# Kernel optimization log

Hardware: AMD Instinct MI355X
Metric: run time of the kernel (lower is better)

## Reference

```python
import math
import jax, jax.numpy as jnp
import numpy as np

D_MODEL = 512
NHEAD = 8
D_HEAD = D_MODEL // NHEAD
ATTN_TEMP = 1.0
B, LQ, LK = 2, 2048, 4096


def _linear_params(key, d_in, d_out):
    kw, kb = jax.random.split(key)
    bound = 1.0 / math.sqrt(d_in)
    W = jax.random.uniform(kw, (d_out, d_in), jnp.float32, -bound, bound)
    b = jax.random.uniform(kb, (d_out,), jnp.float32, -bound, bound)
    return W, b


def setup_inputs() -> dict:
    key = jax.random.key(0)
    ks = jax.random.split(key, 8)
    q = jax.random.normal(ks[0], (B, LQ, D_MODEL), jnp.float32)
    kv = jax.random.normal(ks[1], (B, LK, D_MODEL), jnp.float32)
    key_gate = jax.random.uniform(ks[2], (B, LK), jnp.float32)
    key_mask = jax.random.randint(ks[3], (B, LK), 0, 2, jnp.int32)
    Wq, bq = _linear_params(ks[4], D_MODEL, D_MODEL)
    Wk, bk = _linear_params(ks[5], D_MODEL, D_MODEL)
    Wv, bv = _linear_params(ks[6], D_MODEL, D_MODEL)
    Wo, bo = _linear_params(ks[7], D_MODEL, D_MODEL)
    return {"q": q, "kv": kv, "key_gate": key_gate, "key_mask": key_mask,
            "Wq": Wq, "bq": bq, "Wk": Wk, "bk": bk,
            "Wv": Wv, "bv": bv, "Wo": Wo, "bo": bo}


def reference(q, kv, key_gate, key_mask, Wq, bq, Wk, bk, Wv, bv, Wo, bo):
    Bq, Lq, _ = q.shape
    _, Lk, _ = kv.shape
    # projections -> (B, H, L, Dh)
    qp = (q @ Wq.T + bq).reshape(Bq, Lq, NHEAD, D_HEAD).transpose(0, 2, 1, 3)
    kp = (kv @ Wk.T + bk).reshape(Bq, Lk, NHEAD, D_HEAD).transpose(0, 2, 1, 3)
    vp = (kv @ Wv.T + bv).reshape(Bq, Lk, NHEAD, D_HEAD).transpose(0, 2, 1, 3)
    # scores: (B, H, Lq, Lk)
    scores = jnp.einsum('bhqd,bhkd->bhqk', qp, kp) / (math.sqrt(D_HEAD) * ATTN_TEMP)
    log_gate = jnp.log(jnp.clip(key_gate, 1e-6, None))  # (B, Lk)
    scores = scores + log_gate[:, None, None, :]
    pad = (key_mask == 0)[:, None, None, :]
    scores = jnp.where(pad, -jnp.inf, scores)
    attn = jax.nn.softmax(scores, axis=-1)  # dropout is identity in eval
    out = jnp.einsum('bhqk,bhkd->bhqd', attn, vp)
    out = out.transpose(0, 2, 1, 3).reshape(Bq, Lq, D_MODEL)
    return out @ Wo.T + bo
```

## Files before the change

### kernel.cpp

```cpp
#include <hip/hip_runtime.h>
#include <hip/hip_bf16.h>


using bf16   = __hip_bfloat16;
using bf16x8 = __attribute__((ext_vector_type(8))) short;
using f32x4  = __attribute__((ext_vector_type(4))) float;
using f32x16 = __attribute__((ext_vector_type(16))) float;
using uint4v = __attribute__((ext_vector_type(4))) unsigned int;

#define MFMA16(a, b, c) __builtin_amdgcn_mfma_f32_16x16x32_bf16((a), (b), (c), 0, 0, 0)
#define MFMA32(a, b, c) __builtin_amdgcn_mfma_f32_32x32x16_bf16((a), (b), (c), 0, 0, 0)

__device__ __forceinline__ bf16x8 load8(const bf16* p) {
    return *reinterpret_cast<const bf16x8*>(p);
}
__device__ __forceinline__ unsigned short f2bf(float x) {
    bf16 h = __float2bfloat16(x);
    return *reinterpret_cast<unsigned short*>(&h);
}

__global__ void cvt_all(const float* __restrict__ q, const float* __restrict__ kv,
                        const float* __restrict__ Wq, const float* __restrict__ Wk,
                        const float* __restrict__ Wv, const float* __restrict__ Wo,
                        const float* __restrict__ gate, const int* __restrict__ mask,
                        bf16* __restrict__ qb, bf16* __restrict__ kvb,
                        bf16* __restrict__ Wqb, bf16* __restrict__ Wkb,
                        bf16* __restrict__ Wvb, bf16* __restrict__ Wob,
                        float* __restrict__ g2) {
    const int i = blockIdx.x * 256 + threadIdx.x;
    if (i < 1835008) {
        const float* src; bf16* dst; int j;
        if (i < 524288)       { src = q;  dst = qb;  j = i; }
        else if (i < 1572864) { src = kv; dst = kvb; j = i - 524288; }
        else {
            const int i2 = i - 1572864;
            const int t = i2 >> 16; j = i2 & 65535;
            src = (t == 0) ? Wq : (t == 1) ? Wk : (t == 2) ? Wv : Wo;
            dst = (t == 0) ? Wqb : (t == 1) ? Wkb : (t == 2) ? Wvb : Wob;
        }
        float4 v = reinterpret_cast<const float4*>(src)[j];
        ushort4 o;
        o.x = f2bf(v.x); o.y = f2bf(v.y); o.z = f2bf(v.z); o.w = f2bf(v.w);
        reinterpret_cast<ushort4*>(dst)[j] = o;
    } else {
        const int u = i - 1835008;
        float4 gv = reinterpret_cast<const float4*>(gate)[u];
        int4   mv = reinterpret_cast<const int4*>(mask)[u];
        float4 o;
        o.x = mv.x ? log2f(fmaxf(gv.x, 1e-6f)) : -1e30f;
        o.y = mv.y ? log2f(fmaxf(gv.y, 1e-6f)) : -1e30f;
        o.z = mv.z ? log2f(fmaxf(gv.z, 1e-6f)) : -1e30f;
        o.w = mv.w ? log2f(fmaxf(gv.w, 1e-6f)) : -1e30f;
        reinterpret_cast<float4*>(g2)[u] = o;
    }
}

__device__ __forceinline__ void proj_body(const bf16* __restrict__ X,
                                          const bf16* __restrict__ W,
                                          const float* __restrict__ bias,
                                          void* __restrict__ Cout,
                                          int mode, int L, int mb, int nb,
                                          bf16* Ws) {
    const int tid  = threadIdx.x;
    const int wave = tid >> 6;
    const int lane = tid & 63;
    const int li   = lane & 15;
    const int quad = lane >> 4;
    const int n0   = nb * 64;
    const int m0   = mb * 128 + wave * 32;

    f32x4 zero = {0.f, 0.f, 0.f, 0.f};
    f32x4 acc[2][4];
    for (int mt = 0; mt < 2; ++mt)
        for (int t = 0; t < 4; ++t) acc[mt][t] = zero;

    const bf16* x0 = X + (size_t)(m0 + li) * 512;
    const bf16* x1 = X + (size_t)(m0 + 16 + li) * 512;

    for (int p = 0; p < 2; ++p) {
        __syncthreads();
        for (int i = 0; i < 8; ++i) {
            const int c  = i * 256 + tid;
            const int cr = c >> 5;
            const int kc = (c & 31) * 8;
            *reinterpret_cast<bf16x8*>(&Ws[cr * 264 + kc]) =
                load8(W + (size_t)(n0 + cr) * 512 + p * 256 + kc);
        }
        __syncthreads();

        for (int k0 = 0; k0 < 256; k0 += 32) {
            bf16x8 a0 = load8(x0 + p * 256 + k0 + quad * 8);
            bf16x8 a1 = load8(x1 + p * 256 + k0 + quad * 8);
            for (int t = 0; t < 4; ++t) {
                bf16x8 w8 = load8(&Ws[(t * 16 + li) * 264 + k0 + quad * 8]);
                acc[0][t] = MFMA16(a0, w8, acc[0][t]);
                acc[1][t] = MFMA16(a1, w8, acc[1][t]);
            }
        }
    }

    if (mode == 0) {
        for (int t = 0; t < 4; ++t) {
            const int col = n0 + t * 16 + li;
            const float bcol = bias[col];
            for (int mt = 0; mt < 2; ++mt)
                for (int r = 0; r < 4; ++r) {
                    const int row = m0 + mt * 16 + quad * 4 + r;
                    ((float*)Cout)[(size_t)row * 512 + col] = acc[mt][t][r] + bcol;
                }
        }
    } else {
        __syncthreads();
        bf16* slab = Ws + wave * 2048;
        #pragma unroll
        for (int t = 0; t < 4; ++t) {
            const float bcol = bias[n0 + t * 16 + li];
            #pragma unroll
            for (int mt = 0; mt < 2; ++mt)
                #pragma unroll
                for (int r = 0; r < 4; ++r) {
                    const float v = acc[mt][t][r] + bcol;
                    int lidx;
                    if (mode == 1)
                        lidx = (mt * 16 + quad * 4 + r) * 64 + t * 16 + li;
                    else if (mode == 3)
                        lidx = t * 512 + (li >> 3) * 256 + (mt * 16 + quad * 4 + r) * 8 + (li & 7);
                    else
                        lidx = (t >> 1) * 1024 + mt * 512 + (quad >> 1) * 256
                             + ((t & 1) * 16 + li) * 8 + (quad & 1) * 4 + r;
                    slab[lidx] = __float2bfloat16(v);
                }
        }
        __syncthreads();
        const int bb2 = m0 / L;
        const int i0  = m0 - bb2 * L;
        const int hh  = n0 >> 6;
        const int bh  = bb2 * 8 + hh;
        bf16* base;
        if (mode == 1) base = (bf16*)Cout + ((size_t)bh * L + i0) * 64;
        else           base = (bf16*)Cout + (size_t)bh * L * 64 + (size_t)(i0 >> 5) * 2048;
        #pragma unroll
        for (int s = 0; s < 4; ++s)
            *reinterpret_cast<bf16x8*>(base + s * 512 + lane * 8) =
                load8(&slab[s * 512 + lane * 8]);
    }
}

__global__ void proj_qkv(const bf16* __restrict__ qb, const bf16* __restrict__ kvb,
                         const bf16* __restrict__ Wq, const float* __restrict__ bq,
                         const bf16* __restrict__ Wk, const float* __restrict__ bk,
                         const bf16* __restrict__ Wv, const float* __restrict__ bv,
                         bf16* __restrict__ qp, bf16* __restrict__ kf,
                         bf16* __restrict__ vf) {
    __shared__ alignas(16) bf16 Ws[64 * 264];
    const int l   = blockIdx.x;
    const int w   = l & 63;
    const int myy = (l >> 6) * 8 + (w & 7);
    const int nb  = w >> 3;
    if (myy < 32)      proj_body(qb,  Wq, bq, qp, 1, 2048, myy,      nb, Ws);
    else if (myy < 96) proj_body(kvb, Wk, bk, kf, 3, 4096, myy - 32, nb, Ws);
    else               proj_body(kvb, Wv, bv, vf, 4, 4096, myy - 96, nb, Ws);
}

__global__ void proj_o(const bf16* __restrict__ op, const bf16* __restrict__ Wo,
                       const float* __restrict__ bo, float* __restrict__ out) {
    __shared__ alignas(16) bf16 Ws[64 * 264];
    const int l = blockIdx.x;
    const int w = l & 63;
    proj_body(op, Wo, bo, out, 0, 1, (l >> 6) * 8 + (w & 7), w >> 3, Ws);
}

template<int SP>
__global__ __launch_bounds__(256, 2)
void attn_kernel(const bf16* __restrict__ qp, const bf16* __restrict__ kf,
                 const bf16* __restrict__ vf, const float* __restrict__ g2,
                 float* __restrict__ Opart, float* __restrict__ lpart) {
    constexpr int NT    = 128 / SP;
    constexpr int SLICE = 262144 / SP;
    const int tid  = threadIdx.x;
    const int wave = tid >> 6;
    const int lane = tid & 63;
    const int ql   = lane & 31;
    const int hi   = lane >> 5;

    const int id = blockIdx.x;
    const int qt = (id >> 3) & 7;
    const int gg = ((id >> 6) << 3) | (id & 7);
    const int bh = gg / SP;
    const int sp = gg % SP;
    const int b  = bh >> 3;
    const int q0 = qt * 256 + wave * 64;

    bf16x8 bq[2][4];
    const bf16* qbp = qp + ((size_t)bh * 2048 + q0 + ql) * 64 + hi * 8;
    #pragma unroll
    for (int sub = 0; sub < 2; ++sub)
        #pragma unroll
        for (int ds = 0; ds < 4; ++ds)
            bq[sub][ds] = load8(qbp + sub * 2048 + ds * 16);

    f32x16 od[2][2];
    #pragma unroll
    for (int sub = 0; sub < 2; ++sub)
        #pragma unroll
        for (int t = 0; t < 2; ++t)
            #pragma unroll
            for (int r = 0; r < 16; ++r) od[sub][t][r] = 0.f;
    float lsum[2] = {0.f, 0.f};

    const bf16* kbase = kf + (size_t)bh * 262144 + (size_t)sp * SLICE + lane * 8;
    const bf16* vbase = vf + (size_t)bh * 262144 + (size_t)sp * SLICE + lane * 8;
    const float* gbase = g2 + (size_t)b * 4096 + sp * (4096 / SP) + hi * 4;

    const float SC = 0.18033688011112042f;

    bf16x8 ka0 = load8(kbase);
    bf16x8 ka1 = load8(kbase + 512);
    bf16x8 ka2 = load8(kbase + 1024);
    bf16x8 ka3 = load8(kbase + 1536);

    for (int kt = 0; kt < NT; ++kt) {
        const bf16* vp = vbase + (size_t)kt * 2048;
        bf16x8 bv00 = load8(vp);
        bf16x8 bv01 = load8(vp + 512);
        bf16x8 bv10 = load8(vp + 1024);
        bf16x8 bv11 = load8(vp + 1536);
        const float* gp = gbase + kt * 32;
        f32x4 gv0 = *(const f32x4*)(gp);
        f32x4 gv1 = *(const f32x4*)(gp + 8);
        f32x4 gv2 = *(const f32x4*)(gp + 16);
        f32x4 gv3 = *(const f32x4*)(gp + 24);

        f32x16 s0, s1;
        #pragma unroll
        for (int r = 0; r < 16; ++r) { s0[r] = 0.f; s1[r] = 0.f; }
        __builtin_amdgcn_s_setprio(1);
        s0 = MFMA32(ka0, bq[0][0], s0);
        s0 = MFMA32(ka1, bq[0][1], s0);
        s0 = MFMA32(ka2, bq[0][2], s0);
        s0 = MFMA32(ka3, bq[0][3], s0);
        s1 = MFMA32(ka0, bq[1][0], s1);
        s1 = MFMA32(ka1, bq[1][1], s1);
        s1 = MFMA32(ka2, bq[1][2], s1);
        s1 = MFMA32(ka3, bq[1][3], s1);
        __builtin_amdgcn_s_setprio(0);

        const int ktn = kt < NT - 1 ? kt + 1 : NT - 1;
        const bf16* kp_n = kbase + (size_t)ktn * 2048;
        bf16x8 kn0 = load8(kp_n);
        bf16x8 kn1 = load8(kp_n + 512);
        bf16x8 kn2 = load8(kp_n + 1024);
        bf16x8 kn3 = load8(kp_n + 1536);

        bf16x8 pa00, pa01, pa10, pa11;
        auto softmax = [&](const f32x16& sacc, float& lacc, bf16x8& plo, bf16x8& phi) {
            float p[16];
            #pragma unroll
            for (int r = 0; r < 16; ++r) {
                const float gl = (r < 4) ? gv0[r & 3] : (r < 8) ? gv1[r & 3]
                               : (r < 12) ? gv2[r & 3] : gv3[r & 3];
                p[r] = __builtin_amdgcn_exp2f(fmaf(sacc[r], SC, gl));
            }
            unsigned w[8];
            #pragma unroll
            for (int i = 0; i < 8; ++i)
                asm("v_cvt_pk_bf16_f32 %0, %1, %2"
                    : "=v"(w[i]) : "v"(p[2 * i]), "v"(p[2 * i + 1]));
            #pragma unroll
            for (int st = 1; st < 16; st <<= 1)
                #pragma unroll
                for (int r = 0; r < 16; r += 2 * st) p[r] += p[r + st];
            lacc += p[0];
            asm("v_permlane32_swap_b32 %0, %1" : "+v"(w[0]), "+v"(w[2]));
            asm("v_permlane32_swap_b32 %0, %1" : "+v"(w[1]), "+v"(w[3]));
            asm("v_permlane32_swap_b32 %0, %1" : "+v"(w[4]), "+v"(w[6]));
            asm("v_permlane32_swap_b32 %0, %1" : "+v"(w[5]), "+v"(w[7]));
            uint4v u0 = {w[0], w[1], w[2], w[3]};
            uint4v u1 = {w[4], w[5], w[6], w[7]};
            plo = __builtin_bit_cast(bf16x8, u0);
            phi = __builtin_bit_cast(bf16x8, u1);
        };
        softmax(s0, lsum[0], pa00, pa01);
        softmax(s1, lsum[1], pa10, pa11);

        __builtin_amdgcn_s_setprio(1);
        od[0][0] = MFMA32(pa00, bv00, od[0][0]);
        od[0][0] = MFMA32(pa01, bv01, od[0][0]);
        od[0][1] = MFMA32(pa00, bv10, od[0][1]);
        od[0][1] = MFMA32(pa01, bv11, od[0][1]);
        od[1][0] = MFMA32(pa10, bv00, od[1][0]);
        od[1][0] = MFMA32(pa11, bv01, od[1][0]);
        od[1][1] = MFMA32(pa10, bv10, od[1][1]);
        od[1][1] = MFMA32(pa11, bv11, od[1][1]);
        __builtin_amdgcn_s_setprio(0);

        ka0 = kn0; ka1 = kn1; ka2 = kn2; ka3 = kn3;
    }

    float l0 = lsum[0] + __shfl_xor(lsum[0], 32);
    float l1 = lsum[1] + __shfl_xor(lsum[1], 32);

    float* ob = Opart + ((size_t)(bh * 2048 + q0) * SP + sp) * 64;
    #pragma unroll
    for (int sub = 0; sub < 2; ++sub)
        #pragma unroll
        for (int t = 0; t < 2; ++t)
            #pragma unroll
            for (int r = 0; r < 16; ++r) {
                const int qq = sub * 32 + (r & 3) + 8 * (r >> 2) + hi * 4;
                ob[(size_t)qq * (64 * SP) + t * 32 + ql] = od[sub][t][r];
            }
    if (lane < 32) {
        lpart[((size_t)(bh * 2048 + q0 + lane)) * SP + sp]      = l0;
        lpart[((size_t)(bh * 2048 + q0 + 32 + lane)) * SP + sp] = l1;
    }
}

template<int SP>
__global__ void attn_combine(const float* __restrict__ Opart,
                             const float* __restrict__ lpart,
                             bf16* __restrict__ op) {
    const int gidx = blockIdx.x * 256 + threadIdx.x;
    const int row  = gidx >> 2;
    const int c0   = (gidx & 3) * 16;

    float acc[16];
    #pragma unroll
    for (int j = 0; j < 16; ++j) acc[j] = 0.f;
    float L = 0.f;
    #pragma unroll
    for (int s = 0; s < SP; ++s) {
        const float* src = Opart + ((size_t)row * SP + s) * 64 + c0;
        const float4 v0 = reinterpret_cast<const float4*>(src)[0];
        const float4 v1 = reinterpret_cast<const float4*>(src)[1];
        const float4 v2 = reinterpret_cast<const float4*>(src)[2];
        const float4 v3 = reinterpret_cast<const float4*>(src)[3];
        acc[0] += v0.x; acc[1] += v0.y; acc[2]  += v0.z; acc[3]  += v0.w;
        acc[4] += v1.x; acc[5] += v1.y; acc[6]  += v1.z; acc[7]  += v1.w;
        acc[8] += v2.x; acc[9] += v2.y; acc[10] += v2.z; acc[11] += v2.w;
        acc[12] += v3.x; acc[13] += v3.y; acc[14] += v3.z; acc[15] += v3.w;
        L += lpart[(size_t)row * SP + s];
    }
    const float invL = 1.0f / L;

    const int bh = row >> 11;
    const int q  = row & 2047;
    const int bb = bh >> 3;
    const int hh = bh & 7;
    bf16* dst = op + ((size_t)bb * 2048 + q) * 512 + hh * 64 + c0;
    bf16x8 r0, r1;
    #pragma unroll
    for (int j = 0; j < 8; ++j) {
        r0[j] = f2bf(acc[j] * invL);
        r1[j] = f2bf(acc[8 + j] * invL);
    }
    *reinterpret_cast<bf16x8*>(dst)     = r0;
    *reinterpret_cast<bf16x8*>(dst + 8) = r1;
}

extern "C" void kernel_launch(void* const* d_in, const int* in_sizes, int n_in,
                              void* d_out, int out_size, void* d_ws, size_t ws_size,
                              hipStream_t stream) {
    const float* q    = (const float*)d_in[0];
    const float* kv   = (const float*)d_in[1];
    const float* gate = (const float*)d_in[2];
    const int*   mask = (const int*)d_in[3];
    const float* Wq = (const float*)d_in[4];  const float* bq = (const float*)d_in[5];
    const float* Wk = (const float*)d_in[6];  const float* bk = (const float*)d_in[7];
    const float* Wv = (const float*)d_in[8];  const float* bv = (const float*)d_in[9];
    const float* Wo = (const float*)d_in[10]; const float* bo = (const float*)d_in[11];
    float* out = (float*)d_out;

    char* ws = (char*)d_ws;
    float* g2  = (float*)ws;
    bf16* Wqb  = (bf16*)(ws + (1u  << 20));
    bf16* Wkb  = (bf16*)(ws + (1u  << 20) + (512u << 10));
    bf16* Wvb  = (bf16*)(ws + (2u  << 20));
    bf16* Wob  = (bf16*)(ws + (2u  << 20) + (512u << 10));
    bf16* qb   = (bf16*)(ws + (3u  << 20));
    bf16* kvb  = (bf16*)(ws + (7u  << 20));
    bf16* qp   = (bf16*)(ws + (15u << 20));
    bf16* kf   = (bf16*)(ws + (19u << 20));
    bf16* vf   = (bf16*)(ws + (27u << 20));
    bf16* op   = (bf16*)(ws + (35u << 20));
    float* Opart = (float*)(ws + (39u << 20));

    const bool sp8 = ws_size >= (104ull << 20);
    float* lpart = (float*)(ws + ((size_t)(39u + (sp8 ? 64u : 32u)) << 20));

    cvt_all<<<7176, 256, 0, stream>>>(q, kv, Wq, Wk, Wv, Wo, gate, mask,
                                      qb, kvb, Wqb, Wkb, Wvb, Wob, g2);

    proj_qkv<<<1280, 256, 0, stream>>>(qb, kvb, Wqb, bq, Wkb, bk,
                                       Wvb, bv, qp, kf, vf);

    if (sp8) {
        attn_kernel<8><<<1024, 256, 0, stream>>>(qp, kf, vf, g2, Opart, lpart);
        attn_combine<8><<<512, 256, 0, stream>>>(Opart, lpart, op);
    } else {
        attn_kernel<4><<<512, 256, 0, stream>>>(qp, kf, vf, g2, Opart, lpart);
        attn_combine<4><<<512, 256, 0, stream>>>(Opart, lpart, op);
    }

    proj_o<<<256, 256, 0, stream>>>(op, Wob, bo, out);
}
```

Baseline: 196.2 us.

## Load projection weights directly to registers with prefetch; fix attention split at 4

The projection GEMM stops staging W tiles in shared memory behind block barriers. Each wave now loads its A and W fragments straight from global memory, prefetching the next k-step while the current MFMAs run, and LDS is kept only as a per-wave epilogue slab. The attention split is also fixed at SP=4 instead of picking SP=8 when the workspace is large enough. The trade-off is more redundant global/L2 traffic for W, since each wave fetches its own copy, and possibly lower attention parallelism if SP=8 was being used before.

```diff
diff --git a/kernel.cpp b/kernel.cpp
--- a/kernel.cpp
+++ b/kernel.cpp
@@ -60,7 +60,7 @@
                                           const float* __restrict__ bias,
                                           void* __restrict__ Cout,
                                           int mode, int L, int mb, int nb,
-                                          bf16* Ws) {
+                                          bf16* slab_base) {
     const int tid  = threadIdx.x;
     const int wave = tid >> 6;
     const int lane = tid & 63;
@@ -74,29 +74,37 @@
     for (int mt = 0; mt < 2; ++mt)
         for (int t = 0; t < 4; ++t) acc[mt][t] = zero;
 
-    const bf16* x0 = X + (size_t)(m0 + li) * 512;
-    const bf16* x1 = X + (size_t)(m0 + 16 + li) * 512;
-
-    for (int p = 0; p < 2; ++p) {
-        __syncthreads();
-        for (int i = 0; i < 8; ++i) {
-            const int c  = i * 256 + tid;
-            const int cr = c >> 5;
-            const int kc = (c & 31) * 8;
-            *reinterpret_cast<bf16x8*>(&Ws[cr * 264 + kc]) =
-                load8(W + (size_t)(n0 + cr) * 512 + p * 256 + kc);
-        }
-        __syncthreads();
-
-        for (int k0 = 0; k0 < 256; k0 += 32) {
-            bf16x8 a0 = load8(x0 + p * 256 + k0 + quad * 8);
-            bf16x8 a1 = load8(x1 + p * 256 + k0 + quad * 8);
-            for (int t = 0; t < 4; ++t) {
-                bf16x8 w8 = load8(&Ws[(t * 16 + li) * 264 + k0 + quad * 8]);
-                acc[0][t] = MFMA16(a0, w8, acc[0][t]);
-                acc[1][t] = MFMA16(a1, w8, acc[1][t]);
-            }
-        }
+    const bf16* xp0 = X + (size_t)(m0 + li) * 512 + quad * 8;
+    const bf16* xp1 = xp0 + 16 * 512;
+    const bf16* wp  = W + (size_t)(n0 + li) * 512 + quad * 8;
+
+    bf16x8 a0 = load8(xp0);
+    bf16x8 a1 = load8(xp1);
+    bf16x8 w0 = load8(wp);
+    bf16x8 w1 = load8(wp + 16 * 512);
+    bf16x8 w2 = load8(wp + 32 * 512);
+    bf16x8 w3 = load8(wp + 48 * 512);
+
+    for (int k = 0; k < 512; k += 32) {
+        const int kn = (k < 480) ? k + 32 : k;
+        bf16x8 a0n = load8(xp0 + kn);
+        bf16x8 a1n = load8(xp1 + kn);
+        bf16x8 w0n = load8(wp + kn);
+        bf16x8 w1n = load8(wp + 16 * 512 + kn);
+        bf16x8 w2n = load8(wp + 32 * 512 + kn);
+        bf16x8 w3n = load8(wp + 48 * 512 + kn);
+
+        acc[0][0] = MFMA16(a0, w0, acc[0][0]);
+        acc[1][0] = MFMA16(a1, w0, acc[1][0]);
+        acc[0][1] = MFMA16(a0, w1, acc[0][1]);
+        acc[1][1] = MFMA16(a1, w1, acc[1][1]);
+        acc[0][2] = MFMA16(a0, w2, acc[0][2]);
+        acc[1][2] = MFMA16(a1, w2, acc[1][2]);
+        acc[0][3] = MFMA16(a0, w3, acc[0][3]);
+        acc[1][3] = MFMA16(a1, w3, acc[1][3]);
+
+        a0 = a0n; a1 = a1n;
+        w0 = w0n; w1 = w1n; w2 = w2n; w3 = w3n;
     }
 
     if (mode == 0) {
@@ -110,8 +118,7 @@
                 }
         }
     } else {
-        __syncthreads();
-        bf16* slab = Ws + wave * 2048;
+        bf16* slab = slab_base + wave * 2048;
         #pragma unroll
         for (int t = 0; t < 4; ++t) {
             const float bcol = bias[n0 + t * 16 + li];
@@ -131,7 +138,7 @@
                     slab[lidx] = __float2bfloat16(v);
                 }
         }
-        __syncthreads();
+        __builtin_amdgcn_s_waitcnt(0);
         const int bb2 = m0 / L;
         const int i0  = m0 - bb2 * L;
         const int hh  = n0 >> 6;
@@ -152,22 +159,22 @@
                          const bf16* __restrict__ Wv, const float* __restrict__ bv,
                          bf16* __restrict__ qp, bf16* __restrict__ kf,
                          bf16* __restrict__ vf) {
-    __shared__ alignas(16) bf16 Ws[64 * 264];
+    __shared__ alignas(16) bf16 slab[4 * 2048];
     const int l   = blockIdx.x;
     const int w   = l & 63;
     const int myy = (l >> 6) * 8 + (w & 7);
     const int nb  = w >> 3;
-    if (myy < 32)      proj_body(qb,  Wq, bq, qp, 1, 2048, myy,      nb, Ws);
-    else if (myy < 96) proj_body(kvb, Wk, bk, kf, 3, 4096, myy - 32, nb, Ws);
-    else               proj_body(kvb, Wv, bv, vf, 4, 4096, myy - 96, nb, Ws);
+    if (myy < 32)      proj_body(qb,  Wq, bq, qp, 1, 2048, myy,      nb, slab);
+    else if (myy < 96) proj_body(kvb, Wk, bk, kf, 3, 4096, myy - 32, nb, slab);
+    else               proj_body(kvb, Wv, bv, vf, 4, 4096, myy - 96, nb, slab);
 }
 
 __global__ void proj_o(const bf16* __restrict__ op, const bf16* __restrict__ Wo,
                        const float* __restrict__ bo, float* __restrict__ out) {
-    __shared__ alignas(16) bf16 Ws[64 * 264];
+    __shared__ alignas(16) bf16 slab[4 * 2048];
     const int l = blockIdx.x;
     const int w = l & 63;
-    proj_body(op, Wo, bo, out, 0, 1, (l >> 6) * 8 + (w & 7), w >> 3, Ws);
+    proj_body(op, Wo, bo, out, 0, 1, (l >> 6) * 8 + (w & 7), w >> 3, slab);
 }
 
 template<int SP>
@@ -384,9 +391,7 @@
     bf16* vf   = (bf16*)(ws + (27u << 20));
     bf16* op   = (bf16*)(ws + (35u << 20));
     float* Opart = (float*)(ws + (39u << 20));
-
-    const bool sp8 = ws_size >= (104ull << 20);
-    float* lpart = (float*)(ws + ((size_t)(39u + (sp8 ? 64u : 32u)) << 20));
+    float* lpart = (float*)(ws + (71u << 20));
 
     cvt_all<<<7176, 256, 0, stream>>>(q, kv, Wq, Wk, Wv, Wo, gate, mask,
                                       qb, kvb, Wqb, Wkb, Wvb, Wob, g2);
@@ -394,13 +399,8 @@
     proj_qkv<<<1280, 256, 0, stream>>>(qb, kvb, Wqb, bq, Wkb, bk,
                                        Wvb, bv, qp, kf, vf);
 
-    if (sp8) {
-        attn_kernel<8><<<1024, 256, 0, stream>>>(qp, kf, vf, g2, Opart, lpart);
-        attn_combine<8><<<512, 256, 0, stream>>>(Opart, lpart, op);
-    } else {
-        attn_kernel<4><<<512, 256, 0, stream>>>(qp, kf, vf, g2, Opart, lpart);
-        attn_combine<4><<<512, 256, 0, stream>>>(Opart, lpart, op);
-    }
+    attn_kernel<4><<<512, 256, 0, stream>>>(qp, kf, vf, g2, Opart, lpart);
+    attn_combine<4><<<512, 256, 0, stream>>>(Opart, lpart, op);
 
     proj_o<<<256, 256, 0, stream>>>(op, Wob, bo, out);
 }
```

Result: slower. 215.3 us (+9.7%).

## Fuse fp32-to-bf16 conversion into projection loads and drop the cvt_all kernel

Applied to the files above, without the earlier changes.

Removes the standalone conversion kernel. Projection kernels now read the fp32 inputs and weights directly and convert them to bf16 in registers before the MFMA. The gate/mask log preprocessing moves into extra blocks of the QKV projection launch. This saves one launch and the write and re-read of bf16 copies, but each block now re-converts the weights and reads wider fp32 activations. The attention split is also fixed at 4 instead of picking 8 when workspace allows.

```diff
diff --git a/kernel.cpp b/kernel.cpp
--- a/kernel.cpp
+++ b/kernel.cpp
@@ -18,45 +18,18 @@
     bf16 h = __float2bfloat16(x);
     return *reinterpret_cast<unsigned short*>(&h);
 }
-
-__global__ void cvt_all(const float* __restrict__ q, const float* __restrict__ kv,
-                        const float* __restrict__ Wq, const float* __restrict__ Wk,
-                        const float* __restrict__ Wv, const float* __restrict__ Wo,
-                        const float* __restrict__ gate, const int* __restrict__ mask,
-                        bf16* __restrict__ qb, bf16* __restrict__ kvb,
-                        bf16* __restrict__ Wqb, bf16* __restrict__ Wkb,
-                        bf16* __restrict__ Wvb, bf16* __restrict__ Wob,
-                        float* __restrict__ g2) {
-    const int i = blockIdx.x * 256 + threadIdx.x;
-    if (i < 1835008) {
-        const float* src; bf16* dst; int j;
-        if (i < 524288)       { src = q;  dst = qb;  j = i; }
-        else if (i < 1572864) { src = kv; dst = kvb; j = i - 524288; }
-        else {
-            const int i2 = i - 1572864;
-            const int t = i2 >> 16; j = i2 & 65535;
-            src = (t == 0) ? Wq : (t == 1) ? Wk : (t == 2) ? Wv : Wo;
-            dst = (t == 0) ? Wqb : (t == 1) ? Wkb : (t == 2) ? Wvb : Wob;
-        }
-        float4 v = reinterpret_cast<const float4*>(src)[j];
-        ushort4 o;
-        o.x = f2bf(v.x); o.y = f2bf(v.y); o.z = f2bf(v.z); o.w = f2bf(v.w);
-        reinterpret_cast<ushort4*>(dst)[j] = o;
-    } else {
-        const int u = i - 1835008;
-        float4 gv = reinterpret_cast<const float4*>(gate)[u];
-        int4   mv = reinterpret_cast<const int4*>(mask)[u];
-        float4 o;
-        o.x = mv.x ? log2f(fmaxf(gv.x, 1e-6f)) : -1e30f;
-        o.y = mv.y ? log2f(fmaxf(gv.y, 1e-6f)) : -1e30f;
-        o.z = mv.z ? log2f(fmaxf(gv.z, 1e-6f)) : -1e30f;
-        o.w = mv.w ? log2f(fmaxf(gv.w, 1e-6f)) : -1e30f;
-        reinterpret_cast<float4*>(g2)[u] = o;
-    }
-}
-
-__device__ __forceinline__ void proj_body(const bf16* __restrict__ X,
-                                          const bf16* __restrict__ W,
+__device__ __forceinline__ bf16x8 cvt8(const float4 a, const float4 b) {
+    bf16x8 r;
+    r[0] = (short)f2bf(a.x); r[1] = (short)f2bf(a.y);
+    r[2] = (short)f2bf(a.z); r[3] = (short)f2bf(a.w);
+    r[4] = (short)f2bf(b.x); r[5] = (short)f2bf(b.y);
+    r[6] = (short)f2bf(b.z); r[7] = (short)f2bf(b.w);
+    return r;
+}
+
+template<bool XF32>
+__device__ __forceinline__ void proj_body(const void* __restrict__ X,
+                                          const float* __restrict__ W,
                                           const float* __restrict__ bias,
                                           void* __restrict__ Cout,
                                           int mode, int L, int mb, int nb,
@@ -74,8 +47,10 @@
     for (int mt = 0; mt < 2; ++mt)
         for (int t = 0; t < 4; ++t) acc[mt][t] = zero;
 
-    const bf16* x0 = X + (size_t)(m0 + li) * 512;
-    const bf16* x1 = X + (size_t)(m0 + 16 + li) * 512;
+    const float* xf0 = (const float*)X + (size_t)(m0 + li) * 512 + quad * 8;
+    const float* xf1 = xf0 + 16 * 512;
+    const bf16*  xb0 = (const bf16*)X + (size_t)(m0 + li) * 512 + quad * 8;
+    const bf16*  xb1 = xb0 + 16 * 512;
 
     for (int p = 0; p < 2; ++p) {
         __syncthreads();
@@ -83,14 +58,26 @@
             const int c  = i * 256 + tid;
             const int cr = c >> 5;
             const int kc = (c & 31) * 8;
-            *reinterpret_cast<bf16x8*>(&Ws[cr * 264 + kc]) =
-                load8(W + (size_t)(n0 + cr) * 512 + p * 256 + kc);
+            const float* wsrc = W + (size_t)(n0 + cr) * 512 + p * 256 + kc;
+            const float4 fa = *reinterpret_cast<const float4*>(wsrc);
+            const float4 fb = *reinterpret_cast<const float4*>(wsrc + 4);
+            *reinterpret_cast<bf16x8*>(&Ws[cr * 264 + kc]) = cvt8(fa, fb);
         }
         __syncthreads();
 
         for (int k0 = 0; k0 < 256; k0 += 32) {
-            bf16x8 a0 = load8(x0 + p * 256 + k0 + quad * 8);
-            bf16x8 a1 = load8(x1 + p * 256 + k0 + quad * 8);
+            bf16x8 a0, a1;
+            if constexpr (XF32) {
+                const float* s0 = xf0 + p * 256 + k0;
+                const float* s1 = xf1 + p * 256 + k0;
+                a0 = cvt8(*reinterpret_cast<const float4*>(s0),
+                          *reinterpret_cast<const float4*>(s0 + 4));
+                a1 = cvt8(*reinterpret_cast<const float4*>(s1),
+                          *reinterpret_cast<const float4*>(s1 + 4));
+            } else {
+                a0 = load8(xb0 + p * 256 + k0);
+                a1 = load8(xb1 + p * 256 + k0);
+            }
             for (int t = 0; t < 4; ++t) {
                 bf16x8 w8 = load8(&Ws[(t * 16 + li) * 264 + k0 + quad * 8]);
                 acc[0][t] = MFMA16(a0, w8, acc[0][t]);
@@ -146,28 +133,41 @@
     }
 }
 
-__global__ void proj_qkv(const bf16* __restrict__ qb, const bf16* __restrict__ kvb,
-                         const bf16* __restrict__ Wq, const float* __restrict__ bq,
-                         const bf16* __restrict__ Wk, const float* __restrict__ bk,
-                         const bf16* __restrict__ Wv, const float* __restrict__ bv,
+__global__ void proj_qkv(const float* __restrict__ q, const float* __restrict__ kv,
+                         const float* __restrict__ Wq, const float* __restrict__ bq,
+                         const float* __restrict__ Wk, const float* __restrict__ bk,
+                         const float* __restrict__ Wv, const float* __restrict__ bv,
+                         const float* __restrict__ gate, const int* __restrict__ mask,
                          bf16* __restrict__ qp, bf16* __restrict__ kf,
-                         bf16* __restrict__ vf) {
+                         bf16* __restrict__ vf, float* __restrict__ g2) {
+    if (blockIdx.x >= 1280) {
+        const int u = (blockIdx.x - 1280) * 256 + threadIdx.x;
+        float4 gv = reinterpret_cast<const float4*>(gate)[u];
+        int4   mv = reinterpret_cast<const int4*>(mask)[u];
+        float4 o;
+        o.x = mv.x ? log2f(fmaxf(gv.x, 1e-6f)) : -1e30f;
+        o.y = mv.y ? log2f(fmaxf(gv.y, 1e-6f)) : -1e30f;
+        o.z = mv.z ? log2f(fmaxf(gv.z, 1e-6f)) : -1e30f;
+        o.w = mv.w ? log2f(fmaxf(gv.w, 1e-6f)) : -1e30f;
+        reinterpret_cast<float4*>(g2)[u] = o;
+        return;
+    }
     __shared__ alignas(16) bf16 Ws[64 * 264];
     const int l   = blockIdx.x;
     const int w   = l & 63;
     const int myy = (l >> 6) * 8 + (w & 7);
     const int nb  = w >> 3;
-    if (myy < 32)      proj_body(qb,  Wq, bq, qp, 1, 2048, myy,      nb, Ws);
-    else if (myy < 96) proj_body(kvb, Wk, bk, kf, 3, 4096, myy - 32, nb, Ws);
-    else               proj_body(kvb, Wv, bv, vf, 4, 4096, myy - 96, nb, Ws);
-}
-
-__global__ void proj_o(const bf16* __restrict__ op, const bf16* __restrict__ Wo,
+    if (myy < 32)      proj_body<true>(q,  Wq, bq, qp, 1, 2048, myy,      nb, Ws);
+    else if (myy < 96) proj_body<true>(kv, Wk, bk, kf, 3, 4096, myy - 32, nb, Ws);
+    else               proj_body<true>(kv, Wv, bv, vf, 4, 4096, myy - 96, nb, Ws);
+}
+
+__global__ void proj_o(const bf16* __restrict__ op, const float* __restrict__ Wo,
                        const float* __restrict__ bo, float* __restrict__ out) {
     __shared__ alignas(16) bf16 Ws[64 * 264];
     const int l = blockIdx.x;
     const int w = l & 63;
-    proj_body(op, Wo, bo, out, 0, 1, (l >> 6) * 8 + (w & 7), w >> 3, Ws);
+    proj_body<false>(op, Wo, bo, out, 0, 1, (l >> 6) * 8 + (w & 7), w >> 3, Ws);
 }
 
 template<int SP>
@@ -373,34 +373,18 @@
 
     char* ws = (char*)d_ws;
     float* g2  = (float*)ws;
-    bf16* Wqb  = (bf16*)(ws + (1u  << 20));
-    bf16* Wkb  = (bf16*)(ws + (1u  << 20) + (512u << 10));
-    bf16* Wvb  = (bf16*)(ws + (2u  << 20));
-    bf16* Wob  = (bf16*)(ws + (2u  << 20) + (512u << 10));
-    bf16* qb   = (bf16*)(ws + (3u  << 20));
-    bf16* kvb  = (bf16*)(ws + (7u  << 20));
     bf16* qp   = (bf16*)(ws + (15u << 20));
     bf16* kf   = (bf16*)(ws + (19u << 20));
     bf16* vf   = (bf16*)(ws + (27u << 20));
     bf16* op   = (bf16*)(ws + (35u << 20));
     float* Opart = (float*)(ws + (39u << 20));
-
-    const bool sp8 = ws_size >= (104ull << 20);
-    float* lpart = (float*)(ws + ((size_t)(39u + (sp8 ? 64u : 32u)) << 20));
-
-    cvt_all<<<7176, 256, 0, stream>>>(q, kv, Wq, Wk, Wv, Wo, gate, mask,
-                                      qb, kvb, Wqb, Wkb, Wvb, Wob, g2);
-
-    proj_qkv<<<1280, 256, 0, stream>>>(qb, kvb, Wqb, bq, Wkb, bk,
-                                       Wvb, bv, qp, kf, vf);
-
-    if (sp8) {
-        attn_kernel<8><<<1024, 256, 0, stream>>>(qp, kf, vf, g2, Opart, lpart);
-        attn_combine<8><<<512, 256, 0, stream>>>(Opart, lpart, op);
-    } else {
-        attn_kernel<4><<<512, 256, 0, stream>>>(qp, kf, vf, g2, Opart, lpart);
-        attn_combine<4><<<512, 256, 0, stream>>>(Opart, lpart, op);
-    }
-
-    proj_o<<<256, 256, 0, stream>>>(op, Wob, bo, out);
-}
+    float* lpart = (float*)(ws + (71u << 20));
+
+    proj_qkv<<<1288, 256, 0, stream>>>(q, kv, Wq, bq, Wk, bk, Wv, bv,
+                                       gate, mask, qp, kf, vf, g2);
+
+    attn_kernel<4><<<512, 256, 0, stream>>>(qp, kf, vf, g2, Opart, lpart);
+    attn_combine<4><<<512, 256, 0, stream>>>(Opart, lpart, op);
+
+    proj_o<<<256, 256, 0, stream>>>(op, Wo, bo, out);
+}
```

Result: no change. 200.1 us (+2.0%).

## Fuse split-K attention combine into attention kernel via last-block counter

Applied to the files above, without the earlier changes.

Drops the separate attn_combine launch. Each attention block now increments an atomic counter per (head, query-tile), and the last of the SP split blocks sums the partial outputs and normalisers and writes the bf16 output. It also hard-codes SP=4 instead of choosing SP=8 when the workspace is large enough. This saves one kernel launch and its dependency gap, at the cost of a serialized tail reduction in the last block and less parallelism when SP=8 would have been used.

```diff
diff --git a/kernel.cpp b/kernel.cpp
--- a/kernel.cpp
+++ b/kernel.cpp
@@ -26,7 +26,7 @@
                         bf16* __restrict__ qb, bf16* __restrict__ kvb,
                         bf16* __restrict__ Wqb, bf16* __restrict__ Wkb,
                         bf16* __restrict__ Wvb, bf16* __restrict__ Wob,
-                        float* __restrict__ g2) {
+                        float* __restrict__ g2, int* __restrict__ cnt) {
     const int i = blockIdx.x * 256 + threadIdx.x;
     if (i < 1835008) {
         const float* src; bf16* dst; int j;
@@ -44,6 +44,7 @@
         reinterpret_cast<ushort4*>(dst)[j] = o;
     } else {
         const int u = i - 1835008;
+        if (u < 128) cnt[u] = 0;
         float4 gv = reinterpret_cast<const float4*>(gate)[u];
         int4   mv = reinterpret_cast<const int4*>(mask)[u];
         float4 o;
@@ -174,7 +175,8 @@
 __global__ __launch_bounds__(256, 2)
 void attn_kernel(const bf16* __restrict__ qp, const bf16* __restrict__ kf,
                  const bf16* __restrict__ vf, const float* __restrict__ g2,
-                 float* __restrict__ Opart, float* __restrict__ lpart) {
+                 float* __restrict__ Opart, float* __restrict__ lpart,
+                 int* __restrict__ cnt, bf16* __restrict__ op) {
     constexpr int NT    = 128 / SP;
     constexpr int SLICE = 262144 / SP;
     const int tid  = threadIdx.x;
@@ -314,48 +316,52 @@
         lpart[((size_t)(bh * 2048 + q0 + lane)) * SP + sp]      = l0;
         lpart[((size_t)(bh * 2048 + q0 + 32 + lane)) * SP + sp] = l1;
     }
-}
-
-template<int SP>
-__global__ void attn_combine(const float* __restrict__ Opart,
-                             const float* __restrict__ lpart,
-                             bf16* __restrict__ op) {
-    const int gidx = blockIdx.x * 256 + threadIdx.x;
-    const int row  = gidx >> 2;
-    const int c0   = (gidx & 3) * 16;
-
-    float acc[16];
-    #pragma unroll
-    for (int j = 0; j < 16; ++j) acc[j] = 0.f;
-    float L = 0.f;
-    #pragma unroll
-    for (int s = 0; s < SP; ++s) {
-        const float* src = Opart + ((size_t)row * SP + s) * 64 + c0;
-        const float4 v0 = reinterpret_cast<const float4*>(src)[0];
-        const float4 v1 = reinterpret_cast<const float4*>(src)[1];
-        const float4 v2 = reinterpret_cast<const float4*>(src)[2];
-        const float4 v3 = reinterpret_cast<const float4*>(src)[3];
-        acc[0] += v0.x; acc[1] += v0.y; acc[2]  += v0.z; acc[3]  += v0.w;
-        acc[4] += v1.x; acc[5] += v1.y; acc[6]  += v1.z; acc[7]  += v1.w;
-        acc[8] += v2.x; acc[9] += v2.y; acc[10] += v2.z; acc[11] += v2.w;
-        acc[12] += v3.x; acc[13] += v3.y; acc[14] += v3.z; acc[15] += v3.w;
-        L += lpart[(size_t)row * SP + s];
-    }
-    const float invL = 1.0f / L;
-
-    const int bh = row >> 11;
-    const int q  = row & 2047;
-    const int bb = bh >> 3;
+
+    __threadfence();
+    __syncthreads();
+    __shared__ int is_last;
+    if (tid == 0)
+        is_last = (atomicAdd(&cnt[bh * 8 + qt], 1) == SP - 1);
+    __syncthreads();
+    if (!is_last) return;
+    __threadfence();
+
     const int hh = bh & 7;
-    bf16* dst = op + ((size_t)bb * 2048 + q) * 512 + hh * 64 + c0;
-    bf16x8 r0, r1;
-    #pragma unroll
-    for (int j = 0; j < 8; ++j) {
-        r0[j] = f2bf(acc[j] * invL);
-        r1[j] = f2bf(acc[8 + j] * invL);
-    }
-    *reinterpret_cast<bf16x8*>(dst)     = r0;
-    *reinterpret_cast<bf16x8*>(dst + 8) = r1;
+    for (int u = tid; u < 1024; u += 256) {
+        const int lrow = u >> 2;
+        const int c0   = (u & 3) * 16;
+        const int qq   = qt * 256 + lrow;
+        const size_t row = (size_t)bh * 2048 + qq;
+
+        float acc[16];
+        #pragma unroll
+        for (int j = 0; j < 16; ++j) acc[j] = 0.f;
+        float L = 0.f;
+        #pragma unroll
+        for (int s = 0; s < SP; ++s) {
+            const float* src = Opart + ((size_t)row * SP + s) * 64 + c0;
+            const float4 v0 = reinterpret_cast<const float4*>(src)[0];
+            const float4 v1 = reinterpret_cast<const float4*>(src)[1];
+            const float4 v2 = reinterpret_cast<const float4*>(src)[2];
+            const float4 v3 = reinterpret_cast<const float4*>(src)[3];
+            acc[0] += v0.x; acc[1] += v0.y; acc[2]  += v0.z; acc[3]  += v0.w;
+            acc[4] += v1.x; acc[5] += v1.y; acc[6]  += v1.z; acc[7]  += v1.w;
+            acc[8] += v2.x; acc[9] += v2.y; acc[10] += v2.z; acc[11] += v2.w;
+            acc[12] += v3.x; acc[13] += v3.y; acc[14] += v3.z; acc[15] += v3.w;
+            L += lpart[(size_t)row * SP + s];
+        }
+        const float invL = 1.0f / L;
+
+        bf16* dst = op + ((size_t)b * 2048 + qq) * 512 + hh * 64 + c0;
+        bf16x8 r0, r1;
+        #pragma unroll
+        for (int j = 0; j < 8; ++j) {
+            r0[j] = f2bf(acc[j] * invL);
+            r1[j] = f2bf(acc[8 + j] * invL);
+        }
+        *reinterpret_cast<bf16x8*>(dst)     = r0;
+        *reinterpret_cast<bf16x8*>(dst + 8) = r1;
+    }
 }
 
 extern "C" void kernel_launch(void* const* d_in, const int* in_sizes, int n_in,
@@ -384,23 +390,17 @@
     bf16* vf   = (bf16*)(ws + (27u << 20));
     bf16* op   = (bf16*)(ws + (35u << 20));
     float* Opart = (float*)(ws + (39u << 20));
-
-    const bool sp8 = ws_size >= (104ull << 20);
-    float* lpart = (float*)(ws + ((size_t)(39u + (sp8 ? 64u : 32u)) << 20));
+    float* lpart = (float*)(ws + (71u << 20));
+    int*   cnt   = (int*)(ws + (71u << 20) + (512u << 10));
 
     cvt_all<<<7176, 256, 0, stream>>>(q, kv, Wq, Wk, Wv, Wo, gate, mask,
-                                      qb, kvb, Wqb, Wkb, Wvb, Wob, g2);
+                                      qb, kvb, Wqb, Wkb, Wvb, Wob, g2, cnt);
 
     proj_qkv<<<1280, 256, 0, stream>>>(qb, kvb, Wqb, bq, Wkb, bk,
                                        Wvb, bv, qp, kf, vf);
 
-    if (sp8) {
-        attn_kernel<8><<<1024, 256, 0, stream>>>(qp, kf, vf, g2, Opart, lpart);
-        attn_combine<8><<<512, 256, 0, stream>>>(Opart, lpart, op);
-    } else {
-        attn_kernel<4><<<512, 256, 0, stream>>>(qp, kf, vf, g2, Opart, lpart);
-        attn_combine<4><<<512, 256, 0, stream>>>(Opart, lpart, op);
-    }
+    attn_kernel<4><<<512, 256, 0, stream>>>(qp, kf, vf, g2, Opart, lpart,
+                                            cnt, op);
 
     proj_o<<<256, 256, 0, stream>>>(op, Wob, bo, out);
 }
```

Result: slower. 267.2 us (+36.2%).
